# Performance work log

Hardware: AMD Instinct MI355X
Metric: run time of the kernel (lower is better)

Reference implementation:

```python
import jax, jax.numpy as jnp
import numpy as np

B, S, D = 4, 2048, 1024
N_HEAD = 16
HEAD_DIM = D // N_HEAD


def setup_inputs() -> dict:
    key = jax.random.key(0)
    k1, k2, k3 = jax.random.split(key, 3)
    std = 0.02
    return {
        "x": jax.random.normal(k1, (B, S, D), dtype=jnp.float32),
        "c_attn_w": jax.random.normal(k2, (D, 3 * D), dtype=jnp.float32) * std,
        "c_attn_b": jnp.zeros((3 * D,), dtype=jnp.float32),
        "c_proj_w": jax.random.normal(k3, (D, D), dtype=jnp.float32) * std,
        "c_proj_b": jnp.zeros((D,), dtype=jnp.float32),
    }


def _split_heads(t):
    # [B, S, D] -> [B, H, S, hd]
    b, s, d = t.shape
    return t.reshape(b, s, N_HEAD, d // N_HEAD).transpose(0, 2, 1, 3)


def reference(x, c_attn_w, c_attn_b, c_proj_w, c_proj_b):
    # fused QKV projection (TFConv1D = x @ w + b)
    qkv = x @ c_attn_w + c_attn_b                      # [B, S, 3D]
    q, k, v = jnp.split(qkv, 3, axis=2)
    q, k, v = _split_heads(q), _split_heads(k), _split_heads(v)  # [B, H, S, hd]

    # scaled scores
    w = jnp.einsum('bhqd,bhkd->bhqk', q, k)
    w = w / jnp.sqrt(jnp.asarray(HEAD_DIM, w.dtype))

    # causal mask via multiplicative trick: i >= j - ns + nd (nd == ns == S)
    nd = ns = S
    i = jnp.arange(nd)[:, None]
    j = jnp.arange(ns)[None, :]
    b = (i >= j - ns + nd).astype(w.dtype)[None, None]  # [1,1,nd,ns]
    w = w * b - 10000.0 * (1.0 - b)

    w = jax.nn.softmax(w, axis=-1)
    a = jnp.einsum('bhqk,bhkd->bhqd', w, v)            # [B, H, S, hd]

    # merge heads: [B, H, S, hd] -> [B, S, D]
    a = a.transpose(0, 2, 1, 3).reshape(x.shape[0], x.shape[1], -1)
    a = a @ c_proj_w + c_proj_b
    return a
```

## Files before the change

### kernel.cpp

```cpp
#include <hip/hip_runtime.h>
#include <hip/hip_bf16.h>

typedef unsigned short ushort_t;
typedef __attribute__((ext_vector_type(8))) short short8;
typedef __attribute__((ext_vector_type(4))) float floatx4;

#define LOG2E 1.4426950408889634f

__device__ __forceinline__ unsigned short f2bf(float f) {
    unsigned u = __float_as_uint(f);
    u += 0x7FFF + ((u >> 16) & 1);
    return (unsigned short)(u >> 16);
}

__device__ __forceinline__ void async_ld16(const void* gptr, void* lptr) {
    typedef const __attribute__((address_space(1))) unsigned int TG;
    typedef __attribute__((address_space(3))) unsigned int TL;
    __builtin_amdgcn_global_load_lds((TG*)(unsigned long long)gptr,
                                     (TL*)(unsigned)(unsigned long long)lptr,
                                     16, 0, 0);
}

__global__ __launch_bounds__(256) void prep_kernel(const float* __restrict__ x,
                                                   const float* __restrict__ wqkv,
                                                   const float* __restrict__ wproj,
                                                   ushort_t* __restrict__ xb,
                                                   ushort_t* __restrict__ wqkvT,
                                                   ushort_t* __restrict__ wprojT) {
    __shared__ float t[32][33];
    int bx = blockIdx.x;
    if (bx < 8192) {
        int i = bx * 256 + threadIdx.x;
        float4 v = ((const float4*)x)[i];
        unsigned long long r = (unsigned long long)f2bf(v.x)
                             | ((unsigned long long)f2bf(v.y) << 16)
                             | ((unsigned long long)f2bf(v.z) << 32)
                             | ((unsigned long long)f2bf(v.w) << 48);
        ((unsigned long long*)xb)[i] = r;
        return;
    }
    const float* in; ushort_t* out; int R, C, bidx;
    if (bx < 8192 + 3072) { in = wqkv; out = wqkvT; R = 1024; C = 3072; bidx = bx - 8192; }
    else                  { in = wproj; out = wprojT; R = 1024; C = 1024; bidx = bx - 11264; }
    int nbc = C >> 5;
    int bc = bidx % nbc, br = bidx / nbc;
    int tx = threadIdx.x & 31, ty = threadIdx.x >> 5;
    int r0 = br << 5, c0 = bc << 5;
#pragma unroll
    for (int j = 0; j < 4; ++j)
        t[ty + j * 8][tx] = in[(size_t)(r0 + ty + j * 8) * C + c0 + tx];
    __syncthreads();
#pragma unroll
    for (int j = 0; j < 4; ++j)
        out[(size_t)(c0 + ty + j * 8) * R + r0 + tx] = f2bf(t[tx][ty + j * 8]);
}

__global__ __launch_bounds__(1024) void gemm_qkv_kernel(const ushort_t* __restrict__ A,
                                                        const ushort_t* __restrict__ Bt,
                                                        const float* __restrict__ bias,
                                                        ushort_t* __restrict__ qbuf,
                                                        ushort_t* __restrict__ kbuf,
                                                        ushort_t* __restrict__ vtbuf) {
    extern __shared__ __align__(16) ushort_t lds[];

    int bid = blockIdx.x;
    int wg = (bid & 7) * 64 + (bid >> 3);
    int bm = wg & 63, bn = wg >> 6;
    int m0 = bm << 7, n0 = bn * 384;

    int tid = threadIdx.x;
    int wave = tid >> 6, lane = tid & 63;
    int c = lane & 15, g = lane >> 4;
    int wm = wave >> 3, wn = wave & 7;

    int row0 = tid >> 3;
    int sch  = (tid & 7) ^ (row0 & 7);
    size_t aoff = (size_t)(m0 + row0) * 1024 + sch * 8;
    size_t boff = (size_t)(n0 + row0) * 1024 + sch * 8;

    int co0 = (g * 8) ^ ((c & 7) << 3);
    int co1 = co0 ^ 32;

    floatx4 acc[4][3];
    short8 a[4][2], bb[2];
#pragma unroll
    for (int i2 = 0; i2 < 4; ++i2)
#pragma unroll
        for (int j2 = 0; j2 < 3; ++j2) { floatx4 z = {0.f,0.f,0.f,0.f}; acc[i2][j2] = z; }

    auto stA = [&](int t, int buf) {
        async_ld16(A + aoff + (size_t)t * 64, lds + buf * 8192 + tid * 8);
    };
    auto stB = [&](int t, int buf) {
        const ushort_t* s = Bt + boff + (size_t)t * 64;
        ushort_t* d = lds + 16384 + buf * 24576 + tid * 8;
        async_ld16(s, d);
        async_ld16(s + 131072, d + 8192);
        async_ld16(s + 262144, d + 16384);
    };
    auto ld_a = [&](int buf) {
#pragma unroll
        for (int mi = 0; mi < 4; ++mi) {
            int ro = buf * 8192 + (wm * 64 + mi * 16 + c) * 64;
            a[mi][0] = *(const short8*)&lds[ro + co0];
            a[mi][1] = *(const short8*)&lds[ro + co1];
        }
    };
    auto ld_b = [&](int buf, int nii) {
        int ro = 16384 + buf * 24576 + (wn * 48 + nii * 16 + c) * 64;
        bb[0] = *(const short8*)&lds[ro + co0];
        bb[1] = *(const short8*)&lds[ro + co1];
    };
    auto mm = [&](int nii) {
        asm volatile("s_barrier" ::: "memory");
        asm volatile("s_waitcnt lgkmcnt(0)" ::: "memory");
        __builtin_amdgcn_s_setprio(1);
#pragma unroll
        for (int mi = 0; mi < 4; ++mi)
#pragma unroll
            for (int ks = 0; ks < 2; ++ks)
                acc[mi][nii] = __builtin_amdgcn_mfma_f32_16x16x32_bf16(
                    a[mi][ks], bb[ks], acc[mi][nii], 0, 0, 0);
        __builtin_amdgcn_s_setprio(0);
        asm volatile("s_barrier" ::: "memory");
    };

    stA(0, 0); stB(0, 0);
    stA(1, 1); stB(1, 1);
    asm volatile("s_waitcnt vmcnt(4)" ::: "memory");
    asm volatile("s_barrier" ::: "memory");

#pragma unroll 1
    for (int t = 0; t < 14; ++t) {
        int buf = t & 1;
        ld_a(buf); ld_b(buf, 0);
        mm(0);
        ld_b(buf, 1);
        mm(1);
        ld_b(buf, 2);
        stA(t + 2, buf); stB(t + 2, buf);
        asm volatile("s_waitcnt vmcnt(4)" ::: "memory");
        mm(2);
    }
    ld_a(0); ld_b(0, 0);
    mm(0);
    ld_b(0, 1);
    mm(1);
    ld_b(0, 2);
    asm volatile("s_waitcnt vmcnt(0)" ::: "memory");
    mm(2);
    ld_a(1); ld_b(1, 0);
    mm(0);
    ld_b(1, 1);
    mm(1);
    ld_b(1, 2);
    mm(2);

    int b = m0 >> 11, sbase = m0 & 2047;
    float bv[3], scl[3];
    int headf[3], cinh[3], secf[3];
#pragma unroll
    for (int nii = 0; nii < 3; ++nii) {
        int cb = wn * 48 + nii * 16;
        bv[nii]   = bias[n0 + cb + c];
        headf[nii] = cb >> 6;
        cinh[nii]  = (cb & 63) + c;
        secf[nii]  = (n0 + cb) >> 10;
        scl[nii]   = (secf[nii] == 0) ? (0.125f * LOG2E) : 1.0f;
    }

    __syncthreads();

#pragma unroll
    for (int nii = 0; nii < 3; ++nii) {
        if (secf[nii] < 2) {
#pragma unroll
            for (int mi = 0; mi < 4; ++mi)
#pragma unroll
                for (int r = 0; r < 4; ++r) {
                    int row = wm * 64 + mi * 16 + g * 4 + r;
                    lds[headf[nii] * 9216 + row * 72 + cinh[nii]] =
                        f2bf((acc[mi][nii][r] + bv[nii]) * scl[nii]);
                }
        } else {
#pragma unroll
            for (int mi = 0; mi < 4; ++mi) {
                int d = cinh[nii];
                int s0 = wm * 64 + mi * 16 + g * 4;
                unsigned long long pk =
                      (unsigned long long)f2bf(acc[mi][nii][0] + bv[nii])
                    | ((unsigned long long)f2bf(acc[mi][nii][1] + bv[nii]) << 16)
                    | ((unsigned long long)f2bf(acc[mi][nii][2] + bv[nii]) << 32)
                    | ((unsigned long long)f2bf(acc[mi][nii][3] + bv[nii]) << 48);
                *(unsigned long long*)&lds[headf[nii] * 9216 + d * 136 + s0] = pk;
            }
        }
    }
    __syncthreads();

#pragma unroll 1
    for (int hl = 0; hl < 6; ++hl) {
        int colg = n0 + hl * 64;
        int sech = colg >> 10;
        int hg = (colg & 1023) >> 6;
        size_t bh = (size_t)(b * 16 + hg);
        if (sech < 2) {
            int row = tid >> 3, ch = tid & 7;
            ushort_t* dst = (sech == 0 ? qbuf : kbuf) + bh * 131072
                          + (size_t)(sbase + row) * 64 + ch * 8;
            *(short8*)dst = *(const short8*)&lds[hl * 9216 + row * 72 + ch * 8];
        } else {
            int d = tid >> 4, sq = tid & 15;
            ushort_t* dst = vtbuf + bh * 131072 + (size_t)d * 2048 + sbase + sq * 8;
            *(short8*)dst = *(const short8*)&lds[hl * 9216 + d * 136 + sq * 8];
        }
    }
}

__global__ __launch_bounds__(256, 6) void attn_kernel(const ushort_t* __restrict__ qb_,
                                                      const ushort_t* __restrict__ kb_,
                                                      const ushort_t* __restrict__ vtb_,
                                                      ushort_t* __restrict__ aout) {
    __shared__ __align__(16) ushort_t Ks[64 * 68];
    __shared__ __align__(16) ushort_t Vs[64 * 68];
    __shared__ __align__(16) ushort_t Ps[4][16 * 68];
    int bx = blockIdx.x;
    int qb = 31 - (bx >> 6);
    int bhix = bx & 63;
    int b = bhix >> 4, h = bhix & 15;
    int q0 = qb << 6;
    int tid = threadIdx.x, wave = tid >> 6, lane = tid & 63;
    int c = lane & 15, g = lane >> 4;
    size_t bh = (size_t)(b * 16 + h);

    const ushort_t* Qp = qb_ + (bh * 2048 + q0) * 64;
    const ushort_t* Kp = kb_ + bh * 131072;
    const ushort_t* Vp = vtb_ + bh * 131072;

    int qr = wave * 16 + c;
    short8 qf0 = *(const short8*)(Qp + qr * 64 + g * 8);
    short8 qf1 = *(const short8*)(Qp + qr * 64 + 32 + g * 8);

    short8 vones;
#pragma unroll
    for (int j = 0; j < 8; ++j) vones[j] = (short)0x3F80;

    floatx4 o_acc[4];
    floatx4 lacc = {0.f, 0.f, 0.f, 0.f};
#pragma unroll
    for (int nt = 0; nt < 4; ++nt) { floatx4 z = {0.f,0.f,0.f,0.f}; o_acc[nt] = z; }

    short8 kreg[2], vreg[2];
#pragma unroll
    for (int it = 0; it < 2; ++it) {
        int idx = it * 256 + tid;
        kreg[it] = *(const short8*)(Kp + idx * 8);
        vreg[it] = *(const short8*)(Vp + (idx >> 3) * 2048 + (idx & 7) * 8);
    }

    int qg = q0 + wave * 16 + c;
    for (int kt = 0; kt <= qb; ++kt) {
        int kt0 = kt << 6;
        __syncthreads();
#pragma unroll
        for (int it = 0; it < 2; ++it) {
            int idx = it * 256 + tid;
            *(short8*)&Ks[(idx >> 3) * 68 + (idx & 7) * 8] = kreg[it];
            *(short8*)&Vs[(idx >> 3) * 68 + (idx & 7) * 8] = vreg[it];
        }
        __syncthreads();
        if (kt < qb) {
            int s0 = (kt + 1) << 6;
#pragma unroll
            for (int it = 0; it < 2; ++it) {
                int idx = it * 256 + tid;
                kreg[it] = *(const short8*)(Kp + s0 * 64 + idx * 8);
                vreg[it] = *(const short8*)(Vp + (idx >> 3) * 2048 + s0 + (idx & 7) * 8);
            }
        }
        bool diag = (kt == qb);

#pragma unroll
        for (int nt = 0; nt < 4; ++nt) {
            short8 kf0 = *(const short8*)&Ks[(nt * 16 + c) * 68 + g * 8];
            short8 kf1 = *(const short8*)&Ks[(nt * 16 + c) * 68 + 32 + g * 8];
            floatx4 z = {0.f, 0.f, 0.f, 0.f};
            z = __builtin_amdgcn_mfma_f32_16x16x32_bf16(kf0, qf0, z, 0, 0, 0);
            z = __builtin_amdgcn_mfma_f32_16x16x32_bf16(kf1, qf1, z, 0, 0, 0);

            int kpb = kt0 + nt * 16 + g * 4;
            float p[4];
#pragma unroll
            for (int r = 0; r < 4; ++r) {
                float s = z[r];
                if (diag) s = (kpb + r > qg) ? -1e30f : s;
                p[r] = exp2f(s);
            }
            union { unsigned long long u; __hip_bfloat162 h2[2]; } pk;
            pk.h2[0] = __float22bfloat162_rn(make_float2(p[0], p[1]));
            pk.h2[1] = __float22bfloat162_rn(make_float2(p[2], p[3]));
            *(unsigned long long*)&Ps[wave][c * 68 + nt * 16 + g * 4] = pk.u;
        }

#pragma unroll
        for (int ks = 0; ks < 2; ++ks) {
            short8 pf = *(const short8*)&Ps[wave][c * 68 + ks * 32 + g * 8];
            lacc = __builtin_amdgcn_mfma_f32_16x16x32_bf16(pf, vones, lacc, 0, 0, 0);
#pragma unroll
            for (int nt = 0; nt < 4; ++nt) {
                short8 vf = *(const short8*)&Vs[(nt * 16 + c) * 68 + ks * 32 + g * 8];
                o_acc[nt] = __builtin_amdgcn_mfma_f32_16x16x32_bf16(pf, vf, o_acc[nt], 0, 0, 0);
            }
        }
    }

    float inv[4];
#pragma unroll
    for (int r = 0; r < 4; ++r)
        inv[r] = 1.0f / lacc[r];
#pragma unroll
    for (int nt = 0; nt < 4; ++nt)
#pragma unroll
        for (int r = 0; r < 4; ++r) {
            int q = q0 + wave * 16 + g * 4 + r;
            aout[(size_t)(b * 2048 + q) * 1024 + h * 64 + nt * 16 + c] =
                f2bf(o_acc[nt][r] * inv[r]);
        }
}

__global__ __launch_bounds__(1024) void gemm_proj_kernel(const ushort_t* __restrict__ A,
                                                         const ushort_t* __restrict__ Bt,
                                                         const float* __restrict__ bias,
                                                         float* __restrict__ Cout) {
    extern __shared__ __align__(16) ushort_t lds[];

    int bid = blockIdx.x;
    int wg = (bid & 7) * 32 + (bid >> 3);
    int bm = wg & 31, bn = wg >> 5;
    int m0 = bm << 8, n0 = bn << 7;

    int tid = threadIdx.x;
    int wave = tid >> 6, lane = tid & 63;
    int c = lane & 15, g = lane >> 4;
    int wm = wave >> 2, wn = wave & 3;

    int row0 = tid >> 3;
    int sch  = (tid & 7) ^ (row0 & 7);
    size_t aoff = (size_t)(m0 + row0) * 1024 + sch * 8;
    size_t boff = (size_t)(n0 + row0) * 1024 + sch * 8;

    int co0 = (g * 8) ^ ((c & 7) << 3);
    int co1 = co0 ^ 32;

    floatx4 acc[4][2];
    short8 a[4][2], bb[2];
#pragma unroll
    for (int i2 = 0; i2 < 4; ++i2)
#pragma unroll
        for (int j2 = 0; j2 < 2; ++j2) { floatx4 z = {0.f,0.f,0.f,0.f}; acc[i2][j2] = z; }

    auto stA = [&](int t, int buf) {
        const ushort_t* s = A + aoff + (size_t)t * 64;
        ushort_t* d = lds + buf * 16384 + tid * 8;
        async_ld16(s, d);
        async_ld16(s + 131072, d + 8192);
    };
    auto stB = [&](int t, int buf) {
        async_ld16(Bt + boff + (size_t)t * 64, lds + 32768 + buf * 8192 + tid * 8);
    };
    auto ld_a = [&](int buf) {
#pragma unroll
        for (int mi = 0; mi < 4; ++mi) {
            int ro = buf * 16384 + (wm * 64 + mi * 16 + c) * 64;
            a[mi][0] = *(const short8*)&lds[ro + co0];
            a[mi][1] = *(const short8*)&lds[ro + co1];
        }
    };
    auto ld_b = [&](int buf, int nii) {
        int ro = 32768 + buf * 8192 + (wn * 32 + nii * 16 + c) * 64;
        bb[0] = *(const short8*)&lds[ro + co0];
        bb[1] = *(const short8*)&lds[ro + co1];
    };
    auto mm = [&](int nii) {
        asm volatile("s_barrier" ::: "memory");
        asm volatile("s_waitcnt lgkmcnt(0)" ::: "memory");
        __builtin_amdgcn_s_setprio(1);
#pragma unroll
        for (int mi = 0; mi < 4; ++mi)
#pragma unroll
            for (int ks = 0; ks < 2; ++ks)
                acc[mi][nii] = __builtin_amdgcn_mfma_f32_16x16x32_bf16(
                    a[mi][ks], bb[ks], acc[mi][nii], 0, 0, 0);
        __builtin_amdgcn_s_setprio(0);
        asm volatile("s_barrier" ::: "memory");
    };

    stA(0, 0); stB(0, 0);
    stA(1, 1); stB(1, 1);
    asm volatile("s_waitcnt vmcnt(3)" ::: "memory");
    asm volatile("s_barrier" ::: "memory");

#pragma unroll 1
    for (int t = 0; t < 14; ++t) {
        int buf = t & 1;
        ld_a(buf); ld_b(buf, 0);
        mm(0);
        ld_b(buf, 1);
        stA(t + 2, buf); stB(t + 2, buf);
        asm volatile("s_waitcnt vmcnt(3)" ::: "memory");
        mm(1);
    }
    ld_a(0); ld_b(0, 0);
    mm(0);
    ld_b(0, 1);
    asm volatile("s_waitcnt vmcnt(0)" ::: "memory");
    mm(1);
    ld_a(1); ld_b(1, 0);
    mm(0);
    ld_b(1, 1);
    mm(1);

    float bv[2];
#pragma unroll
    for (int nii = 0; nii < 2; ++nii) bv[nii] = bias[n0 + wn * 32 + nii * 16 + c];
#pragma unroll
    for (int mi = 0; mi < 4; ++mi)
#pragma unroll
        for (int nii = 0; nii < 2; ++nii)
#pragma unroll
            for (int r = 0; r < 4; ++r) {
                int row = m0 + wm * 64 + mi * 16 + g * 4 + r;
                int col = n0 + wn * 32 + nii * 16 + c;
                Cout[(size_t)row * 1024 + col] = acc[mi][nii][r] + bv[nii];
            }
}

extern "C" void kernel_launch(void* const* d_in, const int* in_sizes, int n_in,
                              void* d_out, int out_size, void* d_ws, size_t ws_size,
                              hipStream_t stream) {
    const float* x        = (const float*)d_in[0];
    const float* c_attn_w = (const float*)d_in[1];
    const float* c_attn_b = (const float*)d_in[2];
    const float* c_proj_w = (const float*)d_in[3];
    const float* c_proj_b = (const float*)d_in[4];
    float* out = (float*)d_out;

    char* ws = (char*)d_ws;
    ushort_t* xb     = (ushort_t*)(ws);
    ushort_t* wqkvT  = (ushort_t*)(ws + 16777216);
    ushort_t* wprojT = (ushort_t*)(ws + 23068672);
    ushort_t* qbuf   = (ushort_t*)(ws + 25165824);
    ushort_t* kbuf   = (ushort_t*)(ws + 41943040);
    ushort_t* vtbuf  = (ushort_t*)(ws + 58720256);

    static bool s_attr_set = false;
    if (!s_attr_set) {
        (void)hipFuncSetAttribute(reinterpret_cast<const void*>(gemm_qkv_kernel),
                                  hipFuncAttributeMaxDynamicSharedMemorySize, 131072);
        (void)hipFuncSetAttribute(reinterpret_cast<const void*>(gemm_proj_kernel),
                                  hipFuncAttributeMaxDynamicSharedMemorySize, 98304);
        s_attr_set = true;
    }

    prep_kernel<<<12288, 256, 0, stream>>>(x, c_attn_w, c_proj_w, xb, wqkvT, wprojT);
    gemm_qkv_kernel<<<512, 1024, 131072, stream>>>(xb, wqkvT, c_attn_b, qbuf, kbuf, vtbuf);
    attn_kernel<<<2048, 256, 0, stream>>>(qbuf, kbuf, vtbuf, xb);
    gemm_proj_kernel<<<256, 1024, 98304, stream>>>(xb, wprojT, c_proj_b, out);
}
```

Measured before the change: 262.6 us.

## Use 32x32 MFMA in attention with register-resident P and split-K wave reduction

Moves the attention inner loop from 16x16x32 to 32x32x16 bf16 MFMA. Each wave now owns 32 query rows and half of the 64-key tile. Softmax probabilities go from the score accumulator straight into the PV operand through lane shuffles, so the per-wave LDS round-trip for P is gone. The two key halves are merged at the end through an LDS reduction of the partial O and row sums. This cuts LDS traffic and instruction count, but it raises register pressure (launch bounds drop from 6 to 4 blocks) and adds an epilogue reduction with an extra barrier.

After: 255.6 us (median of 2 runs). 1.03x faster.

```diff
diff --git a/kernel.cpp b/kernel.cpp
--- a/kernel.cpp
+++ b/kernel.cpp
@@ -4,6 +4,7 @@
 typedef unsigned short ushort_t;
 typedef __attribute__((ext_vector_type(8))) short short8;
 typedef __attribute__((ext_vector_type(4))) float floatx4;
+typedef __attribute__((ext_vector_type(16))) float floatx16;
 
 #define LOG2E 1.4426950408889634f
 
@@ -217,38 +218,40 @@
     }
 }
 
-__global__ __launch_bounds__(256, 6) void attn_kernel(const ushort_t* __restrict__ qb_,
+__global__ __launch_bounds__(256, 4) void attn_kernel(const ushort_t* __restrict__ qb_,
                                                       const ushort_t* __restrict__ kb_,
                                                       const ushort_t* __restrict__ vtb_,
                                                       ushort_t* __restrict__ aout) {
     __shared__ __align__(16) ushort_t Ks[64 * 68];
     __shared__ __align__(16) ushort_t Vs[64 * 68];
-    __shared__ __align__(16) ushort_t Ps[4][16 * 68];
+    __shared__ __align__(16) float Lo[2][32][64];
+    __shared__ float Ll[2][32];
     int bx = blockIdx.x;
     int qb = 31 - (bx >> 6);
     int bhix = bx & 63;
     int b = bhix >> 4, h = bhix & 15;
     int q0 = qb << 6;
     int tid = threadIdx.x, wave = tid >> 6, lane = tid & 63;
-    int c = lane & 15, g = lane >> 4;
+    int qh = wave >> 1, kh = wave & 1;
+    int l31 = lane & 31, hi = lane >> 5;
     size_t bh = (size_t)(b * 16 + h);
 
-    const ushort_t* Qp = qb_ + (bh * 2048 + q0) * 64;
+    const ushort_t* Qp = qb_ + (bh * 2048 + q0 + qh * 32 + l31) * 64;
     const ushort_t* Kp = kb_ + bh * 131072;
     const ushort_t* Vp = vtb_ + bh * 131072;
 
-    int qr = wave * 16 + c;
-    short8 qf0 = *(const short8*)(Qp + qr * 64 + g * 8);
-    short8 qf1 = *(const short8*)(Qp + qr * 64 + 32 + g * 8);
+    short8 qf[4];
+#pragma unroll
+    for (int s = 0; s < 4; ++s)
+        qf[s] = *(const short8*)(Qp + s * 16 + hi * 8);
 
     short8 vones;
 #pragma unroll
     for (int j = 0; j < 8; ++j) vones[j] = (short)0x3F80;
 
-    floatx4 o_acc[4];
-    floatx4 lacc = {0.f, 0.f, 0.f, 0.f};
-#pragma unroll
-    for (int nt = 0; nt < 4; ++nt) { floatx4 z = {0.f,0.f,0.f,0.f}; o_acc[nt] = z; }
+    floatx16 o0, o1, lacc;
+#pragma unroll
+    for (int i = 0; i < 16; ++i) { o0[i] = 0.f; o1[i] = 0.f; lacc[i] = 0.f; }
 
     short8 kreg[2], vreg[2];
 #pragma unroll
@@ -258,7 +261,8 @@
         vreg[it] = *(const short8*)(Vp + (idx >> 3) * 2048 + (idx & 7) * 8);
     }
 
-    int qg = q0 + wave * 16 + c;
+    int qg = q0 + qh * 32 + l31;
+    int krow = (kh * 32 + l31) * 68 + hi * 8;
     for (int kt = 0; kt <= qb; ++kt) {
         int kt0 = kt << 6;
         __syncthreads();
@@ -280,52 +284,74 @@
         }
         bool diag = (kt == qb);
 
-#pragma unroll
-        for (int nt = 0; nt < 4; ++nt) {
-            short8 kf0 = *(const short8*)&Ks[(nt * 16 + c) * 68 + g * 8];
-            short8 kf1 = *(const short8*)&Ks[(nt * 16 + c) * 68 + 32 + g * 8];
-            floatx4 z = {0.f, 0.f, 0.f, 0.f};
-            z = __builtin_amdgcn_mfma_f32_16x16x32_bf16(kf0, qf0, z, 0, 0, 0);
-            z = __builtin_amdgcn_mfma_f32_16x16x32_bf16(kf1, qf1, z, 0, 0, 0);
-
-            int kpb = kt0 + nt * 16 + g * 4;
-            float p[4];
-#pragma unroll
-            for (int r = 0; r < 4; ++r) {
-                float s = z[r];
-                if (diag) s = (kpb + r > qg) ? -1e30f : s;
-                p[r] = exp2f(s);
+        floatx16 z;
+#pragma unroll
+        for (int i = 0; i < 16; ++i) z[i] = 0.f;
+#pragma unroll
+        for (int s = 0; s < 4; ++s) {
+            short8 kf = *(const short8*)&Ks[krow + s * 16];
+            z = __builtin_amdgcn_mfma_f32_32x32x16_bf16(kf, qf[s], z, 0, 0, 0);
+        }
+
+        int kpb_ = kt0 + kh * 32 + 4 * hi;
+#pragma unroll
+        for (int r = 0; r < 16; ++r) {
+            float s = z[r];
+            if (diag) s = (kpb_ + (r & 3) + 8 * (r >> 2) > qg) ? -1e30f : s;
+            z[r] = exp2f(s);
+        }
+        unsigned w[4][2];
+#pragma unroll
+        for (int t2 = 0; t2 < 4; ++t2)
+#pragma unroll
+            for (int u2 = 0; u2 < 2; ++u2) {
+                union { unsigned u; __hip_bfloat162 h2; } pk;
+                pk.h2 = __float22bfloat162_rn(
+                    make_float2(z[t2 * 4 + u2 * 2], z[t2 * 4 + u2 * 2 + 1]));
+                w[t2][u2] = pk.u;
             }
-            union { unsigned long long u; __hip_bfloat162 h2[2]; } pk;
-            pk.h2[0] = __float22bfloat162_rn(make_float2(p[0], p[1]));
-            pk.h2[1] = __float22bfloat162_rn(make_float2(p[2], p[3]));
-            *(unsigned long long*)&Ps[wave][c * 68 + nt * 16 + g * 4] = pk.u;
-        }
-
-#pragma unroll
-        for (int ks = 0; ks < 2; ++ks) {
-            short8 pf = *(const short8*)&Ps[wave][c * 68 + ks * 32 + g * 8];
-            lacc = __builtin_amdgcn_mfma_f32_16x16x32_bf16(pf, vones, lacc, 0, 0, 0);
-#pragma unroll
-            for (int nt = 0; nt < 4; ++nt) {
-                short8 vf = *(const short8*)&Vs[(nt * 16 + c) * 68 + ks * 32 + g * 8];
-                o_acc[nt] = __builtin_amdgcn_mfma_f32_16x16x32_bf16(pf, vf, o_acc[nt], 0, 0, 0);
-            }
-        }
-    }
-
-    float inv[4];
-#pragma unroll
-    for (int r = 0; r < 4; ++r)
-        inv[r] = 1.0f / lacc[r];
-#pragma unroll
-    for (int nt = 0; nt < 4; ++nt)
-#pragma unroll
-        for (int r = 0; r < 4; ++r) {
-            int q = q0 + wave * 16 + g * 4 + r;
-            aout[(size_t)(b * 2048 + q) * 1024 + h * 64 + nt * 16 + c] =
-                f2bf(o_acc[nt][r] * inv[r]);
-        }
+#pragma unroll
+        for (int s = 0; s < 2; ++s) {
+            unsigned s0w = hi ? w[2 * s][0] : w[2 * s + 1][0];
+            unsigned s1w = hi ? w[2 * s][1] : w[2 * s + 1][1];
+            unsigned r0 = (unsigned)__shfl_xor((int)s0w, 32);
+            unsigned r1 = (unsigned)__shfl_xor((int)s1w, 32);
+            union { unsigned u[4]; short8 v; } pa;
+            if (hi == 0) { pa.u[0] = w[2*s][0]; pa.u[1] = w[2*s][1]; pa.u[2] = r0; pa.u[3] = r1; }
+            else         { pa.u[0] = r0; pa.u[1] = r1; pa.u[2] = w[2*s+1][0]; pa.u[3] = w[2*s+1][1]; }
+            short8 vb0 = *(const short8*)&Vs[l31 * 68 + kh * 32 + s * 16 + hi * 8];
+            short8 vb1 = *(const short8*)&Vs[(32 + l31) * 68 + kh * 32 + s * 16 + hi * 8];
+            o0   = __builtin_amdgcn_mfma_f32_32x32x16_bf16(pa.v, vb0,   o0,   0, 0, 0);
+            o1   = __builtin_amdgcn_mfma_f32_32x32x16_bf16(pa.v, vb1,   o1,   0, 0, 0);
+            lacc = __builtin_amdgcn_mfma_f32_32x32x16_bf16(pa.v, vones, lacc, 0, 0, 0);
+        }
+    }
+
+    if (kh == 1) {
+#pragma unroll
+        for (int r = 0; r < 16; ++r) {
+            int q = (r & 3) + 8 * (r >> 2) + 4 * hi;
+            Lo[qh][q][l31]      = o0[r];
+            Lo[qh][q][32 + l31] = o1[r];
+        }
+        if (l31 == 0) {
+#pragma unroll
+            for (int r = 0; r < 16; ++r)
+                Ll[qh][(r & 3) + 8 * (r >> 2) + 4 * hi] = lacc[r];
+        }
+    }
+    __syncthreads();
+    if (kh == 0) {
+#pragma unroll
+        for (int r = 0; r < 16; ++r) {
+            int q = (r & 3) + 8 * (r >> 2) + 4 * hi;
+            float linv = 1.0f / (lacc[r] + Ll[qh][q]);
+            int qgl = q0 + qh * 32 + q;
+            size_t base = (size_t)(b * 2048 + qgl) * 1024 + h * 64;
+            aout[base + l31]      = f2bf((o0[r] + Lo[qh][q][l31]) * linv);
+            aout[base + 32 + l31] = f2bf((o1[r] + Lo[qh][q][32 + l31]) * linv);
+        }
+    }
 }
 
 __global__ __launch_bounds__(1024) void gemm_proj_kernel(const ushort_t* __restrict__ A,
```
